# Kernel tuning notes

Measured on AMD Instinct MI355X. Metric: run time of the kernel, lower is better.

## Reference

```python
import jax, jax.numpy as jnp
import numpy as np

P = 0.3            # swap probability (matches init_kwargs p)
H = 224
W = 224
PERM_SEED = 42     # fixed key so the reference is deterministic


def _index_permute(key, h, w, p):
    """Sequential random-neighbor swap permutation over an h*w grid.

    Faithful to CLOPLayer._index_permute: visit all flat indices in a random
    order; for each, with prob p swap it with one of its 4 toroidal neighbors
    (each with prob p/4). Implemented as a lax.scan over the visitation order
    (the swaps are inherently sequential / order-dependent).
    """
    n = h * w
    k1, k2 = jax.random.split(key)
    order = jax.random.permutation(k1, n)                       # visitation order
    probs = jnp.array([1.0 - p, p / 4, p / 4, p / 4, p / 4], dtype=jnp.float32)
    rs = jax.random.choice(k2, 5, shape=(n,), p=probs)          # move type per step

    def step(indexes, inp):
        idx, r = inp
        i = idx // w
        j = idx % w
        ip = jnp.where(r == 1, (i + 1) % h, jnp.where(r == 2, (i - 1) % h, i))
        jp = jnp.where(r == 3, (j + 1) % w, jnp.where(r == 4, (j - 1) % w, j))
        idx2 = jnp.where(r == 0, idx, ip * w + jp)              # r==0 -> self-swap (no-op)
        a = indexes[idx]
        b = indexes[idx2]
        indexes = indexes.at[idx].set(b).at[idx2].set(a)
        return indexes, None

    indexes = jnp.arange(n, dtype=jnp.int32)
    indexes, _ = jax.lax.scan(step, indexes, (order.astype(jnp.int32), rs.astype(jnp.int32)))
    return indexes


def setup_inputs() -> dict:
    key = jax.random.key(0)
    x = jax.random.normal(key, (128, 3, H, W), dtype=jnp.float32)
    return {"x": x}


def reference(x) -> jnp.ndarray:
    b, c, h, w = x.shape
    idx = _index_permute(jax.random.key(PERM_SEED), h, w, P)     # [h*w] int32
    flat = x.reshape(b, c, h * w)
    # torch.gather(flat, 2, idx broadcast over b,c) == take along last axis
    res = jnp.take(flat, idx, axis=2)
    return res.reshape(b, c, h, w)
```

## Files before the change

### kernel.cpp

```cpp
#include <hip/hip_runtime.h>
#include <cstdint>
#include <cstring>
#include <vector>
#include <algorithm>


#define PH 224
#define PW 224
#define PN (PH * PW)
#define NBC (128 * 3)

#define R_OUT 32
#define NWIN (PH / R_OUT)
#define KWIN (R_OUT * PW)
#define TPB 512
#define EMIT_IT (KWIN / (2 * TPB))
#define OVF_CAP 1024

typedef float f4v __attribute__((ext_vector_type(4)));
typedef float f2v __attribute__((ext_vector_type(2)));

static inline uint32_t rotl32(uint32_t v, int d) {
  return (v << d) | (v >> (32 - d));
}

static void tf2x32(uint32_t k0, uint32_t k1, uint32_t x0, uint32_t x1,
                   uint32_t& o0, uint32_t& o1) {
  const uint32_t ks0 = k0, ks1 = k1, ks2 = k0 ^ k1 ^ 0x1BD11BDAu;
  uint32_t v0 = x0 + ks0;
  uint32_t v1 = x1 + ks1;
  static const int ra[4] = {13, 15, 26, 6};
  static const int rb[4] = {17, 29, 16, 24};
#define R4X(rr)                             \
  do {                                      \
    for (int _i = 0; _i < 4; ++_i) {        \
      v0 += v1;                             \
      v1 = rotl32(v1, (rr)[_i]);            \
      v1 ^= v0;                             \
    }                                       \
  } while (0)
  R4X(ra); v0 += ks1; v1 += ks2 + 1u;
  R4X(rb); v0 += ks2; v1 += ks0 + 2u;
  R4X(ra); v0 += ks0; v1 += ks1 + 3u;
  R4X(rb); v0 += ks1; v1 += ks2 + 4u;
  R4X(ra); v0 += ks2; v1 += ks0 + 5u;
#undef R4X
  o0 = v0;
  o1 = v1;
}

static void jax_split2(uint32_t k0, uint32_t k1,
                       uint32_t& a0, uint32_t& a1, uint32_t& b0, uint32_t& b1) {
  tf2x32(k0, k1, 0u, 0u, a0, a1);
  tf2x32(k0, k1, 0u, 1u, b0, b1);
}

static inline uint32_t jax_rb32(uint32_t k0, uint32_t k1, uint32_t i) {
  uint32_t y0, y1;
  tf2x32(k0, k1, 0u, i, y0, y1);
  return y0 ^ y1;
}

static std::vector<int> compute_perm() {
  const int n = PN;
  const uint32_t K0 = 0u, K1 = 42u;

  uint32_t k1a, k1b, k2a, k2b;
  jax_split2(K0, K1, k1a, k1b, k2a, k2b);

  std::vector<int> order(n);
  for (int i = 0; i < n; ++i) order[i] = i;
  uint32_t ck0 = k1a, ck1 = k1b;
  std::vector<std::pair<uint32_t, int>> kv(n);
  for (int round = 0; round < 2; ++round) {
    uint32_t nk0, nk1, sk0, sk1;
    jax_split2(ck0, ck1, nk0, nk1, sk0, sk1);
    ck0 = nk0; ck1 = nk1;
    for (int i = 0; i < n; ++i) {
      kv[i] = {jax_rb32(sk0, sk1, (uint32_t)i), order[i]};
    }
    std::stable_sort(kv.begin(), kv.end(),
                     [](const std::pair<uint32_t, int>& a,
                        const std::pair<uint32_t, int>& b) {
                       return a.first < b.first;
                     });
    for (int i = 0; i < n; ++i) order[i] = kv[i].second;
  }

  float probs[5] = {(float)(1.0 - 0.3), (float)(0.3 / 4), (float)(0.3 / 4),
                    (float)(0.3 / 4), (float)(0.3 / 4)};
  float pc[5];
  pc[0] = probs[0];
  for (int i = 1; i < 5; ++i) pc[i] = pc[i - 1] + probs[i];

  std::vector<uint8_t> rs(n);
  for (int i = 0; i < n; ++i) {
    uint32_t bits = jax_rb32(k2a, k2b, (uint32_t)i);
    uint32_t fb = (bits >> 9) | 0x3f800000u;
    float u;
    std::memcpy(&u, &fb, 4);
    u -= 1.0f;
    if (u < 0.0f) u = 0.0f;
    float r = pc[4] * (1.0f - u);
    int ind = (int)(std::lower_bound(pc, pc + 5, r) - pc);
    rs[i] = (uint8_t)ind;
  }

  std::vector<int> idx(n);
  for (int i = 0; i < n; ++i) idx[i] = i;
  for (int t = 0; t < n; ++t) {
    const int id = order[t];
    const int r = rs[t];
    const int i = id / PW, j = id % PW;
    int ip = i, jp = j;
    if (r == 1)      ip = (i + 1) % PH;
    else if (r == 2) ip = (i - 1 + PH) % PH;
    else if (r == 3) jp = (j + 1) % PW;
    else if (r == 4) jp = (j - 1 + PW) % PW;
    const int id2 = (r == 0) ? id : (ip * PW + jp);
    const int a = idx[id];
    const int b = idx[id2];
    idx[id]  = b;
    idx[id2] = a;
  }
  return idx;
}

static bool build_tables(const std::vector<int>& idx, int halo,
                         std::vector<uint16_t>& lofs, std::vector<int>& ovf,
                         std::vector<int>& cnt) {
  const int sr = R_OUT + 2 * halo;
  lofs.assign((size_t)NWIN * KWIN, 0);
  ovf.assign((size_t)NWIN * OVF_CAP, 0);
  cnt.assign(NWIN, 0);
  for (int w = 0; w < NWIN; ++w) {
    const int g0 = w * R_OUT - halo;
    int no = 0;
    for (int kk = 0; kk < KWIN; ++kk) {
      const int k = w * KWIN + kk;
      const int s = idx[k];
      const int srow = s / PW, scol = s % PW;
      int i = ((srow - g0) % PH + PH) % PH;
      if (i < sr) {
        lofs[(size_t)w * KWIN + kk] = (uint16_t)(i * PW + scol);
      } else {
        if (no >= OVF_CAP) return false;
        ovf[(size_t)w * OVF_CAP + no] = s;
        lofs[(size_t)w * KWIN + kk] = (uint16_t)(sr * PW + no);
        ++no;
      }
    }
    cnt[w] = no;
  }
  return true;
}

struct PermHolder {
  std::vector<int> h_idx;
  int* d_idx = nullptr;
  uint16_t* d_lofs = nullptr;
  int* d_ovf = nullptr;
  int* d_cnt = nullptr;
  int halo = 0;

  PermHolder() {
    h_idx = compute_perm();

    int* p = nullptr;
    if (hipMalloc(&p, PN * sizeof(int)) == hipSuccess &&
        hipMemcpy(p, h_idx.data(), PN * sizeof(int),
                  hipMemcpyHostToDevice) == hipSuccess) {
      d_idx = p;
    }

    for (int h : {2, 8}) {
      std::vector<uint16_t> lofs;
      std::vector<int> ovf, cnt;
      if (!build_tables(h_idx, h, lofs, ovf, cnt)) continue;
      uint16_t* ql = nullptr;
      int* qo = nullptr;
      int* qc = nullptr;
      bool ok =
          hipMalloc(&ql, lofs.size() * sizeof(uint16_t)) == hipSuccess &&
          hipMemcpy(ql, lofs.data(), lofs.size() * sizeof(uint16_t),
                    hipMemcpyHostToDevice) == hipSuccess &&
          hipMalloc(&qo, ovf.size() * sizeof(int)) == hipSuccess &&
          hipMemcpy(qo, ovf.data(), ovf.size() * sizeof(int),
                    hipMemcpyHostToDevice) == hipSuccess &&
          hipMalloc(&qc, cnt.size() * sizeof(int)) == hipSuccess &&
          hipMemcpy(qc, cnt.data(), cnt.size() * sizeof(int),
                    hipMemcpyHostToDevice) == hipSuccess;
      if (ok) {
        d_lofs = ql;
        d_ovf = qo;
        d_cnt = qc;
        halo = h;
        break;
      }
    }
  }
};
static PermHolder g_perm;

template <int HALO_T>
__global__ __launch_bounds__(TPB, 8) void clop_lds_t(
    const float* __restrict__ x, const uint16_t* __restrict__ lofs,
    const int* __restrict__ ovf_idx, const int* __restrict__ ovf_cnt,
    float* __restrict__ out) {
  constexpr int SR = R_OUT + 2 * HALO_T;
  constexpr int STAGE = SR * (PW / 4);
  constexpr int SITER = (STAGE + TPB - 1) / TPB;
  __shared__ float tile[SR * PW + OVF_CAP];

  const int w = blockIdx.x;
  const size_t bc = blockIdx.y;
  const int g0 = w * R_OUT - HALO_T;
  const float* xs = x + bc * PN;

#pragma unroll
  for (int i = 0; i < SITER; ++i) {
    const int t = (int)threadIdx.x + i * TPB;
    if (t < STAGE) {
      const int r = t / (PW / 4);
      const int j = (t % (PW / 4)) * 4;
      int g = g0 + r;
      if (g < 0) g += PH;
      else if (g >= PH) g -= PH;
      *(f4v*)(tile + r * PW + j) = *(const f4v*)(xs + g * PW + j);
    }
  }

  const uint32_t* lw2 =
      (const uint32_t*)(lofs + (size_t)w * KWIN);
  uint32_t o2[EMIT_IT];
#pragma unroll
  for (int i = 0; i < EMIT_IT; ++i)
    o2[i] = lw2[i * TPB + (int)threadIdx.x];

  const int novf = ovf_cnt[w];
  for (int t = (int)threadIdx.x; t < novf; t += TPB)
    tile[SR * PW + t] = xs[ovf_idx[w * OVF_CAP + t]];

  __syncthreads();

  float* ob = out + bc * PN + (size_t)w * KWIN;
#pragma unroll
  for (int i = 0; i < EMIT_IT; ++i) {
    const uint32_t o = o2[i];
    f2v v;
    v.x = tile[o & 0xFFFFu];
    v.y = tile[o >> 16];
    __builtin_nontemporal_store(
        v, (f2v*)(ob + i * (2 * TPB) + 2 * (int)threadIdx.x));
  }
}

__global__ __launch_bounds__(256) void clop_gather(
    const float* __restrict__ x, const int* __restrict__ idx,
    float* __restrict__ out) {
  const int k = blockIdx.x * 256 + threadIdx.x;
  const int s = idx[k];
  const size_t bc0 = (size_t)blockIdx.y * 8;
#pragma unroll
  for (int t = 0; t < 8; ++t) {
    const size_t bc = bc0 + t;
    out[bc * PN + k] = x[bc * PN + s];
  }
}

extern "C" void kernel_launch(void* const* d_in, const int* in_sizes, int n_in,
                              void* d_out, int out_size, void* d_ws,
                              size_t ws_size, hipStream_t stream) {
  const float* x = (const float*)d_in[0];
  float* out = (float*)d_out;

  if (g_perm.halo == 2) {
    dim3 grid(NWIN, NBC);
    clop_lds_t<2><<<grid, TPB, 0, stream>>>(x, g_perm.d_lofs, g_perm.d_ovf,
                                            g_perm.d_cnt, out);
    return;
  }
  if (g_perm.halo == 8) {
    dim3 grid(NWIN, NBC);
    clop_lds_t<8><<<grid, TPB, 0, stream>>>(x, g_perm.d_lofs, g_perm.d_ovf,
                                            g_perm.d_cnt, out);
    return;
  }

  const int* idx;
  if (g_perm.d_idx != nullptr) {
    idx = g_perm.d_idx;
  } else {
    (void)hipMemcpyAsync(d_ws, g_perm.h_idx.data(), PN * sizeof(int),
                         hipMemcpyHostToDevice, stream);
    idx = (const int*)d_ws;
  }
  dim3 grid(PN / 256, NBC / 8);
  clop_gather<<<grid, 256, 0, stream>>>(x, idx, out);
}
```

Baseline: 136.5 us.

## Double-buffer LDS tiles with async global_load_lds across persistent tile loop

Each block now processes three consecutive (bc, window) tiles. It stages the next tile into a second LDS buffer with direct global-to-LDS loads while emitting the current tile's permuted outputs. The halo is fixed at 2, and the fallback gather kernel is rewritten to use int4 index loads and vector stores. The aim is to overlap the global-load latency of staging with the LDS gather and store phase. The cost is double the LDS per block, which lowers occupancy, and a third as many blocks.

```diff
diff --git a/kernel.cpp b/kernel.cpp
--- a/kernel.cpp
+++ b/kernel.cpp
@@ -11,11 +11,19 @@
 #define NBC (128 * 3)
 
 #define R_OUT 32
+#define HALO 2
+#define SR (R_OUT + 2 * HALO)
+#define SRPW (SR * PW)
 #define NWIN (PH / R_OUT)
 #define KWIN (R_OUT * PW)
 #define TPB 512
 #define EMIT_IT (KWIN / (2 * TPB))
+#define STAGE_F4 (SR * (PW / 4))
+#define SITER ((STAGE_F4 + TPB - 1) / TPB)
 #define OVF_CAP 1024
+#define NTILES (NBC * NWIN)
+#define TPBLK 3
+#define NBLK (NTILES / TPBLK)
 
 typedef float f4v __attribute__((ext_vector_type(4)));
 typedef float f2v __attribute__((ext_vector_type(2)));
@@ -126,27 +134,26 @@
   return idx;
 }
 
-static bool build_tables(const std::vector<int>& idx, int halo,
+static bool build_tables(const std::vector<int>& idx,
                          std::vector<uint16_t>& lofs, std::vector<int>& ovf,
                          std::vector<int>& cnt) {
-  const int sr = R_OUT + 2 * halo;
   lofs.assign((size_t)NWIN * KWIN, 0);
   ovf.assign((size_t)NWIN * OVF_CAP, 0);
   cnt.assign(NWIN, 0);
   for (int w = 0; w < NWIN; ++w) {
-    const int g0 = w * R_OUT - halo;
+    const int g0 = w * R_OUT - HALO;
     int no = 0;
     for (int kk = 0; kk < KWIN; ++kk) {
       const int k = w * KWIN + kk;
       const int s = idx[k];
       const int srow = s / PW, scol = s % PW;
       int i = ((srow - g0) % PH + PH) % PH;
-      if (i < sr) {
+      if (i < SR) {
         lofs[(size_t)w * KWIN + kk] = (uint16_t)(i * PW + scol);
       } else {
         if (no >= OVF_CAP) return false;
         ovf[(size_t)w * OVF_CAP + no] = s;
-        lofs[(size_t)w * KWIN + kk] = (uint16_t)(sr * PW + no);
+        lofs[(size_t)w * KWIN + kk] = (uint16_t)(SRPW + no);
         ++no;
       }
     }
@@ -161,7 +168,7 @@
   uint16_t* d_lofs = nullptr;
   int* d_ovf = nullptr;
   int* d_cnt = nullptr;
-  int halo = 0;
+  bool lds_ok = false;
 
   PermHolder() {
     h_idx = compute_perm();
@@ -173,10 +180,9 @@
       d_idx = p;
     }
 
-    for (int h : {2, 8}) {
-      std::vector<uint16_t> lofs;
-      std::vector<int> ovf, cnt;
-      if (!build_tables(h_idx, h, lofs, ovf, cnt)) continue;
+    std::vector<uint16_t> lofs;
+    std::vector<int> ovf, cnt;
+    if (build_tables(h_idx, lofs, ovf, cnt)) {
       uint16_t* ql = nullptr;
       int* qo = nullptr;
       int* qc = nullptr;
@@ -194,77 +200,122 @@
         d_lofs = ql;
         d_ovf = qo;
         d_cnt = qc;
-        halo = h;
-        break;
+        lds_ok = true;
       }
     }
   }
 };
 static PermHolder g_perm;
 
-template <int HALO_T>
-__global__ __launch_bounds__(TPB, 8) void clop_lds_t(
-    const float* __restrict__ x, const uint16_t* __restrict__ lofs,
-    const int* __restrict__ ovf_idx, const int* __restrict__ ovf_cnt,
-    float* __restrict__ out) {
-  constexpr int SR = R_OUT + 2 * HALO_T;
-  constexpr int STAGE = SR * (PW / 4);
-  constexpr int SITER = (STAGE + TPB - 1) / TPB;
-  __shared__ float tile[SR * PW + OVF_CAP];
-
-  const int w = blockIdx.x;
-  const size_t bc = blockIdx.y;
-  const int g0 = w * R_OUT - HALO_T;
-  const float* xs = x + bc * PN;
-
+__device__ __forceinline__ void stage_issue(const float* __restrict__ xs,
+                                            float* buf, int w,
+                                            const int* __restrict__ ovf_w,
+                                            int novf) {
+  const int g0 = w * R_OUT - HALO;
 #pragma unroll
   for (int i = 0; i < SITER; ++i) {
     const int t = (int)threadIdx.x + i * TPB;
-    if (t < STAGE) {
+    if (t < STAGE_F4) {
       const int r = t / (PW / 4);
       const int j = (t % (PW / 4)) * 4;
       int g = g0 + r;
       if (g < 0) g += PH;
       else if (g >= PH) g -= PH;
-      *(f4v*)(tile + r * PW + j) = *(const f4v*)(xs + g * PW + j);
-    }
-  }
-
-  const uint32_t* lw2 =
-      (const uint32_t*)(lofs + (size_t)w * KWIN);
-  uint32_t o2[EMIT_IT];
-#pragma unroll
-  for (int i = 0; i < EMIT_IT; ++i)
-    o2[i] = lw2[i * TPB + (int)threadIdx.x];
-
-  const int novf = ovf_cnt[w];
-  for (int t = (int)threadIdx.x; t < novf; t += TPB)
-    tile[SR * PW + t] = xs[ovf_idx[w * OVF_CAP + t]];
-
-  __syncthreads();
-
-  float* ob = out + bc * PN + (size_t)w * KWIN;
-#pragma unroll
-  for (int i = 0; i < EMIT_IT; ++i) {
-    const uint32_t o = o2[i];
-    f2v v;
-    v.x = tile[o & 0xFFFFu];
-    v.y = tile[o >> 16];
-    __builtin_nontemporal_store(
-        v, (f2v*)(ob + i * (2 * TPB) + 2 * (int)threadIdx.x));
-  }
-}
-
-__global__ __launch_bounds__(256) void clop_gather(
+      __builtin_amdgcn_global_load_lds(
+          (const __attribute__((address_space(1))) void*)(xs + g * PW + j),
+          (__attribute__((address_space(3))) void*)(buf + (size_t)t * 4),
+          16, 0, 0);
+    }
+  }
+  for (int t = (int)threadIdx.x; t < novf; t += TPB) {
+    const int s = ovf_w[t];
+    __builtin_amdgcn_global_load_lds(
+        (const __attribute__((address_space(1))) void*)(xs + s),
+        (__attribute__((address_space(3))) void*)(buf + SRPW + t), 4, 0, 0);
+  }
+}
+
+__global__ __launch_bounds__(TPB) void clop_pipe(
+    const float* __restrict__ x, const uint16_t* __restrict__ lofs,
+    const int* __restrict__ ovf_idx, const int* __restrict__ ovf_cnt,
+    float* __restrict__ out) {
+  __shared__ float tile[2][SRPW + OVF_CAP];
+
+  const int t0 = (int)blockIdx.x * TPBLK;
+
+  uint32_t oc[EMIT_IT];
+  {
+    const int w = t0 % NWIN;
+    const size_t bc = t0 / NWIN;
+    stage_issue(x + bc * PN, tile[0], w, ovf_idx + (size_t)w * OVF_CAP,
+                ovf_cnt[w]);
+    const uint32_t* lw2 = (const uint32_t*)(lofs + (size_t)w * KWIN);
+#pragma unroll
+    for (int i = 0; i < EMIT_IT; ++i)
+      oc[i] = lw2[i * TPB + (int)threadIdx.x];
+  }
+  asm volatile("s_waitcnt vmcnt(0)" ::: "memory");
+  __builtin_amdgcn_s_barrier();
+
+  int cur = 0;
+  for (int k = 0; k < TPBLK; ++k) {
+    const int tt = t0 + k;
+    const int w = tt % NWIN;
+    const size_t bc = tt / NWIN;
+
+    uint32_t on[EMIT_IT];
+    if (k + 1 < TPBLK) {
+      const int t2 = tt + 1;
+      const int w2 = t2 % NWIN;
+      const size_t bc2 = t2 / NWIN;
+      stage_issue(x + bc2 * PN, tile[cur ^ 1], w2,
+                  ovf_idx + (size_t)w2 * OVF_CAP, ovf_cnt[w2]);
+      const uint32_t* lw2 = (const uint32_t*)(lofs + (size_t)w2 * KWIN);
+#pragma unroll
+      for (int i = 0; i < EMIT_IT; ++i)
+        on[i] = lw2[i * TPB + (int)threadIdx.x];
+    }
+
+    float* ob = out + bc * PN + (size_t)w * KWIN;
+    const float* tl = tile[cur];
+#pragma unroll
+    for (int i = 0; i < EMIT_IT; ++i) {
+      const uint32_t o = oc[i];
+      f2v v;
+      v.x = tl[o & 0xFFFFu];
+      v.y = tl[o >> 16];
+      __builtin_nontemporal_store(
+          v, (f2v*)(ob + i * (2 * TPB) + 2 * (int)threadIdx.x));
+    }
+
+    asm volatile("s_waitcnt vmcnt(0)" ::: "memory");
+    __builtin_amdgcn_s_barrier();
+#pragma unroll
+    for (int i = 0; i < EMIT_IT; ++i) oc[i] = on[i];
+    cur ^= 1;
+  }
+}
+
+__global__ __launch_bounds__(256) void clop_gather4(
     const float* __restrict__ x, const int* __restrict__ idx,
     float* __restrict__ out) {
-  const int k = blockIdx.x * 256 + threadIdx.x;
-  const int s = idx[k];
-  const size_t bc0 = (size_t)blockIdx.y * 8;
-#pragma unroll
-  for (int t = 0; t < 8; ++t) {
-    const size_t bc = bc0 + t;
-    out[bc * PN + k] = x[bc * PN + s];
+  const int w = blockIdx.x;
+  const size_t bc = blockIdx.y;
+  const int base = w * KWIN;
+  const float* xs = x + bc * PN;
+  float* ob = out + bc * PN + base;
+  const int4* iv = (const int4*)(idx + base);
+
+#pragma unroll
+  for (int i = 0; i < 7; ++i) {
+    const int g = i * 256 + (int)threadIdx.x;
+    const int4 s = iv[g];
+    f4v v;
+    v.x = xs[s.x];
+    v.y = xs[s.y];
+    v.z = xs[s.z];
+    v.w = xs[s.w];
+    __builtin_nontemporal_store(v, (f4v*)(ob + (size_t)g * 4));
   }
 }
 
@@ -274,16 +325,9 @@
   const float* x = (const float*)d_in[0];
   float* out = (float*)d_out;
 
-  if (g_perm.halo == 2) {
-    dim3 grid(NWIN, NBC);
-    clop_lds_t<2><<<grid, TPB, 0, stream>>>(x, g_perm.d_lofs, g_perm.d_ovf,
-                                            g_perm.d_cnt, out);
-    return;
-  }
-  if (g_perm.halo == 8) {
-    dim3 grid(NWIN, NBC);
-    clop_lds_t<8><<<grid, TPB, 0, stream>>>(x, g_perm.d_lofs, g_perm.d_ovf,
-                                            g_perm.d_cnt, out);
+  if (g_perm.lds_ok) {
+    clop_pipe<<<dim3(NBLK), TPB, 0, stream>>>(x, g_perm.d_lofs, g_perm.d_ovf,
+                                              g_perm.d_cnt, out);
     return;
   }
 
@@ -295,6 +339,6 @@
                          hipMemcpyHostToDevice, stream);
     idx = (const int*)d_ws;
   }
-  dim3 grid(PN / 256, NBC / 8);
-  clop_gather<<<grid, 256, 0, stream>>>(x, idx, out);
-}
+  dim3 grid(NWIN, NBC);
+  clop_gather4<<<grid, 256, 0, stream>>>(x, idx, out);
+}
```

Result: no change. 137.4 us (+0.7%).
